# Performance work log

Hardware: AMD Instinct MI355X
Metric: run time of the kernel (lower is better)

The kernel has to match this reference:

```python
import jax, jax.numpy as jnp
import numpy as np

HID = 768
NSPLITS = 12
HEAD_RATIO = 2
H = NSPLITS // HEAD_RATIO          # 6 attention heads
D = HID // NSPLITS                 # 64 head size
AH = H * D                         # 384 all_head_size
KS = 9                             # conv kernel size
PAD = (KS - 1) // 2
B, S = 4, 1024


def setup_inputs() -> dict:
    key = jax.random.key(0)
    ks = jax.random.split(key, 16)
    std = 0.02
    inp = {
        "Q": jax.random.normal(ks[0], (B, S, HID), jnp.float32),
        "K": jax.random.normal(ks[1], (B, S, HID), jnp.float32),
        "V": jax.random.normal(ks[2], (B, S, HID), jnp.float32),
        "td": jax.random.uniform(ks[3], (B, S), jnp.float32),
        "mask": jax.random.randint(ks[4], (B, S), 0, 2, jnp.int32),
        # projection weights, applied as x @ W (in, out)
        "Wq": jax.random.normal(ks[5], (HID, AH), jnp.float32) * std,
        "Wk": jax.random.normal(ks[6], (HID, AH), jnp.float32) * std,
        "Wv": jax.random.normal(ks[7], (HID, AH), jnp.float32) * std,
        # separable conv: depthwise (HID, KS), pointwise (AH, HID), bias (AH,)
        "dw_w": jax.random.normal(ks[8], (HID, KS), jnp.float32) * std,
        "pw_w": jax.random.normal(ks[9], (AH, HID), jnp.float32) * std,
        "sep_b": jnp.zeros((AH,), jnp.float32),
        # conv_kernel_layer Linear(AH -> H*KS)
        "ck_W": jax.random.normal(ks[10], (AH, H * KS), jnp.float32) * std,
        "ck_b": jnp.zeros((H * KS,), jnp.float32),
        # conv_out_layer Linear(HID -> AH)
        "co_W": jax.random.normal(ks[11], (HID, AH), jnp.float32) * std,
        "co_b": jnp.zeros((AH,), jnp.float32),
        # gammas init to zeros as in torch module
        "gammas": jnp.zeros((H, 1, 1), jnp.float32),
    }
    return inp


def dist_func(scores, td, am, gammas):
    # scores: [B,H,S,S]; am: [B,1,1,S] bool key mask; entirely non-differentiable.
    s = scores.shape[-1]
    dt = scores.dtype
    amf = am.astype(dt)
    p = jax.nn.softmax(jnp.where(am, scores, -1e8), axis=-1) * amf
    distcum = jnp.cumsum(p, axis=-1)
    disttotal = jnp.sum(p, axis=-1, keepdims=True)
    # |j - i| position distance
    pos = jnp.abs(jnp.arange(s)[None, :] - jnp.arange(s)[:, None]).astype(dt)
    dist_scores = jnp.sqrt(jnp.clip((disttotal - distcum) * pos[None, None], 0.0, None))
    gamma = -jax.nn.softplus(gammas)[None]  # (1,H,1,1)
    total_effect = jnp.clip(jnp.exp(dist_scores * gamma), 1e-5, 1e5)
    # time-distance effect on strictly-lower-triangular positions
    tdn = td / jnp.maximum(jnp.linalg.norm(td, axis=-1, keepdims=True), 1e-12)
    td_scores = jnp.broadcast_to(tdn[:, None, None, :], scores.shape)
    td_sm = jax.nn.softmax(jnp.where(am, td_scores, -1e4), axis=-1)
    lower = jnp.tril(jnp.ones((s, s), dt), -1)  # (triu == 0)
    return jax.lax.stop_gradient(total_effect - td_sm * lower[None, None])


def reference(Q, K, V, td, mask, Wq, Wk, Wv, dw_w, pw_w, sep_b, ck_W, ck_b, co_W, co_b, gammas):
    b, s, hid = Q.shape
    mq = Q @ Wq  # (B,S,AH)
    mk = K @ Wk
    mv = V @ Wv
    # SeparableConv1D over sequence dim of K
    x = jnp.transpose(K, (0, 2, 1))  # (B,HID,S)
    dw = jax.lax.conv_general_dilated(
        x, dw_w[:, None, :], window_strides=(1,), padding=[(PAD, PAD)],
        feature_group_count=hid, dimension_numbers=("NCH", "OIH", "NCH"))
    pw = jnp.einsum("bcs,oc->bos", dw, pw_w) + sep_b[None, :, None]
    mkc = jnp.transpose(pw, (0, 2, 1))  # (B,S,AH)

    q = mq.reshape(b, s, H, D).transpose(0, 2, 1, 3)
    k = mk.reshape(b, s, H, D).transpose(0, 2, 1, 3)
    v = mv.reshape(b, s, H, D).transpose(0, 2, 1, 3)

    # dynamic span convolution
    conv_attn = mkc * mq                                   # (B,S,AH)
    ck = (conv_attn @ ck_W + ck_b).reshape(b, s, H, KS)
    ck = jax.nn.softmax(ck, axis=-1)                       # per-position kernel
    co = V @ co_W + co_b                                   # (B,S,AH)
    co_pad = jnp.pad(co, ((0, 0), (PAD, PAD), (0, 0)))
    idx = jnp.arange(s)[:, None] + jnp.arange(KS)[None, :]  # (S,KS)
    unf = co_pad[:, idx, :].reshape(b, s, KS, H, D)         # sliding window gather
    conv_out = jnp.einsum("bskhd,bshk->bshd", unf, ck)      # (B,S,H,D)

    # attention with distance decay
    scores = jnp.einsum("bhid,bhjd->bhij", q, k) / np.float32(np.sqrt(D))
    am = (mask[:, None, None, :] != 0)  # (B,1,1,S) key mask
    total_effect = dist_func(scores, td, am, gammas)
    scores = jnp.where(am, scores * total_effect, -1e8)
    probs = jax.nn.softmax(scores, axis=-1)
    ctx = jnp.einsum("bhij,bhjd->bhid", probs, v).transpose(0, 2, 1, 3)  # (B,S,H,D)

    out = jnp.concatenate([ctx, conv_out], axis=2).reshape(b, s, HEAD_RATIO * AH)
    return out
```

## Files before the change

kernel.cpp:

```cpp
#include <hip/hip_runtime.h>
#include <hip/hip_bf16.h>

#define HIDC 768
#define Hh   6
#define Dd   64
#define AHc  384
#define KSc  9
#define PADc 4
#define Bb   4
#define Ss   1024
#define MRr  (Bb * Ss)

typedef __attribute__((ext_vector_type(8))) __bf16 bf16x8;
typedef __attribute__((ext_vector_type(4))) float  f32x4;

__device__ __forceinline__ void split8(const float* p, bf16x8& hi, bf16x8& lo) {
    float4 x0 = *(const float4*)p;
    float4 x1 = *(const float4*)(p + 4);
    float xs[8] = {x0.x, x0.y, x0.z, x0.w, x1.x, x1.y, x1.z, x1.w};
#pragma unroll
    for (int e = 0; e < 8; ++e) {
        __bf16 hv = (__bf16)xs[e];
        hi[e] = hv;
        lo[e] = (__bf16)(xs[e] - (float)hv);
    }
}

__device__ __forceinline__ void split8r(const float* xs, bf16x8& hi, bf16x8& lo) {
#pragma unroll
    for (int e = 0; e < 8; ++e) {
        __bf16 hv = (__bf16)xs[e];
        hi[e] = hv;
        lo[e] = (__bf16)(xs[e] - (float)hv);
    }
}

__device__ __forceinline__ bf16x8 cvt8(const float* p) {
    float4 x0 = *(const float4*)p;
    float4 x1 = *(const float4*)(p + 4);
    float xs[8] = {x0.x, x0.y, x0.z, x0.w, x1.x, x1.y, x1.z, x1.w};
    bf16x8 h;
#pragma unroll
    for (int e = 0; e < 8; ++e) h[e] = (__bf16)xs[e];
    return h;
}

__global__ void k_depthwise(const float* __restrict__ Kin, const float* __restrict__ dww,
                            float* __restrict__ dwseq) {
    int idx = blockIdx.x * 256 + threadIdx.x;
    if (idx >= Bb * Ss * HIDC / 4) return;
    int c4 = idx % (HIDC / 4);
    int s  = (idx / (HIDC / 4)) % Ss;
    int b  = idx / ((HIDC / 4) * Ss);
    int c  = c4 * 4;
    float wv[4][KSc];
#pragma unroll
    for (int j = 0; j < 4; ++j)
#pragma unroll
        for (int k = 0; k < KSc; ++k) wv[j][k] = dww[(c + j) * KSc + k];
    float4 acc = {0.f, 0.f, 0.f, 0.f};
#pragma unroll
    for (int k = 0; k < KSc; ++k) {
        int sp = s + k - PADc;
        if (sp >= 0 && sp < Ss) {
            float4 v = *(const float4*)&Kin[(size_t)(b * Ss + sp) * HIDC + c];
            acc.x += v.x * wv[0][k]; acc.y += v.y * wv[1][k];
            acc.z += v.z * wv[2][k]; acc.w += v.w * wv[3][k];
        }
    }
    *(float4*)&dwseq[(size_t)idx * 4] = acc;
}

__global__ __launch_bounds__(256) void k_wsplit_t(const float* __restrict__ Wq, const float* __restrict__ Wk,
                                                  const float* __restrict__ Wv, const float* __restrict__ coW,
                                                  __bf16* __restrict__ Whi, __bf16* __restrict__ Wlo) {
    int z = blockIdx.z;
    const float* src = (z == 0) ? Wq : (z == 1) ? Wk : (z == 2) ? Wv : coW;
    int n0 = blockIdx.x * 64, k0 = blockIdx.y * 64;
    int tid = threadIdx.x;
    int r = tid >> 2, cq = tid & 3;
    __shared__ float tile[64][65];
#pragma unroll
    for (int e = 0; e < 4; ++e) {
        float4 v = *(const float4*)&src[(size_t)(k0 + r) * AHc + n0 + cq * 16 + e * 4];
        tile[r][cq * 16 + e * 4 + 0] = v.x;
        tile[r][cq * 16 + e * 4 + 1] = v.y;
        tile[r][cq * 16 + e * 4 + 2] = v.z;
        tile[r][cq * 16 + e * 4 + 3] = v.w;
    }
    __syncthreads();
    float x[16];
#pragma unroll
    for (int e = 0; e < 16; ++e) x[e] = tile[cq * 16 + e][r];
    bf16x8 h0, l0, h1, l1;
    split8r(x, h0, l0);
    split8r(x + 8, h1, l1);
    size_t dst = ((size_t)(z * AHc + n0 + r)) * HIDC + k0 + cq * 16;
    *(bf16x8*)(Whi + dst)     = h0;
    *(bf16x8*)(Whi + dst + 8) = h1;
    *(bf16x8*)(Wlo + dst)     = l0;
    *(bf16x8*)(Wlo + dst + 8) = l1;
}

__global__ void k_wsplit_c(const float* __restrict__ pww,
                           __bf16* __restrict__ Whi, __bf16* __restrict__ Wlo) {
    int idx = blockIdx.x * 256 + threadIdx.x;
    if (idx >= AHc * HIDC / 8) return;
    bf16x8 hi, lo;
    split8(pww + (size_t)idx * 8, hi, lo);
    size_t dst = (size_t)4 * AHc * HIDC + (size_t)idx * 8;
    *(bf16x8*)(Whi + dst) = hi;
    *(bf16x8*)(Wlo + dst) = lo;
}

__global__ void k_qkvsplit(const float* __restrict__ mq, const float* __restrict__ mk,
                           __bf16* __restrict__ qh, __bf16* __restrict__ kh,
                           __bf16* __restrict__ kl) {
    const int n8 = MRr * AHc / 8;
    int idx = blockIdx.x * 256 + threadIdx.x;
    if (idx >= 2 * n8) return;
    int which = idx / n8, i8 = idx % n8;
    if (which == 0) {
        *(bf16x8*)(qh + (size_t)i8 * 8) = cvt8(mq + (size_t)i8 * 8);
    } else {
        bf16x8 hi, lo;
        split8(mk + (size_t)i8 * 8, hi, lo);
        *(bf16x8*)(kh + (size_t)i8 * 8) = hi;
        *(bf16x8*)(kl + (size_t)i8 * 8) = lo;
    }
}

__global__ __launch_bounds__(256) void k_vtrans(const float* __restrict__ mv,
                                                __bf16* __restrict__ vt) {
    int s0 = blockIdx.x * 64;
    int h = blockIdx.y % Hh, b = blockIdx.y / Hh;
    int tid = threadIdx.x;
    int r = tid >> 2, cq = tid & 3;
    __shared__ float tile[64][65];
    const float* src = mv + (size_t)(b * Ss + s0 + r) * AHc + h * Dd + cq * 16;
#pragma unroll
    for (int e = 0; e < 4; ++e) {
        float4 v = *(const float4*)(src + e * 4);
        tile[r][cq * 16 + e * 4 + 0] = v.x;
        tile[r][cq * 16 + e * 4 + 1] = v.y;
        tile[r][cq * 16 + e * 4 + 2] = v.z;
        tile[r][cq * 16 + e * 4 + 3] = v.w;
    }
    __syncthreads();
    bf16x8 o0, o1;
#pragma unroll
    for (int e = 0; e < 8; ++e) {
        o0[e] = (__bf16)tile[cq * 16 + e][r];
        o1[e] = (__bf16)tile[cq * 16 + 8 + e][r];
    }
    __bf16* dst = vt + ((size_t)((b * Hh + h) * Dd + r)) * Ss + s0 + cq * 16;
    *(bf16x8*)dst       = o0;
    *(bf16x8*)(dst + 8) = o1;
}

__global__ void k_bias(const float* __restrict__ cob, const float* __restrict__ sepb,
                       float* __restrict__ biasb) {
    int idx = blockIdx.x * 256 + threadIdx.x;
    if (idx >= 5 * AHc) return;
    int z = idx / AHc, n = idx % AHc;
    biasb[idx] = (z == 3) ? cob[n] : (z == 4) ? sepb[n] : 0.f;
}

__global__ __launch_bounds__(256) void k_gemm5(
        const float* __restrict__ Q, const float* __restrict__ Kin,
        const float* __restrict__ V, const float* __restrict__ dwseq,
        const __bf16* __restrict__ Whi, const __bf16* __restrict__ Wlo,
        const float* __restrict__ biasb, float* __restrict__ Call) {
    __shared__ __attribute__((aligned(16))) __bf16 As_hi[128 * 40];
    __shared__ __attribute__((aligned(16))) __bf16 Bs_hi[128 * 40];
    __shared__ __attribute__((aligned(16))) __bf16 Bs_lo[128 * 40];

    int z = blockIdx.z;
    const float* Asrc = (z == 0) ? Q : (z == 1) ? Kin : (z <= 3) ? V : dwseq;
    int m0 = blockIdx.y * 128, n0 = blockIdx.x * 128;
    int tid = threadIdx.x;
    int wave = tid >> 6, lane = tid & 63, quad = lane >> 4, l15 = lane & 15;

    int sr = tid >> 1;
    int sk = (tid & 1) * 16;
    const float* Arow = Asrc + (size_t)(m0 + sr) * HIDC + sk;
    const __bf16* BhiRow = Whi + ((size_t)(z * AHc + n0 + sr)) * HIDC + sk;
    const __bf16* BloRow = Wlo + ((size_t)(z * AHc + n0 + sr)) * HIDC + sk;

    f32x4 acc[4][4] = {};

    for (int k0 = 0; k0 < HIDC; k0 += 32) {
        const float* ap = Arow + k0;
        *(bf16x8*)&As_hi[sr * 40 + sk]     = cvt8(ap);
        *(bf16x8*)&As_hi[sr * 40 + sk + 8] = cvt8(ap + 8);
        {
            const __bf16* bh = BhiRow + k0;
            const __bf16* bl = BloRow + k0;
            *(bf16x8*)&Bs_hi[sr * 40 + sk]     = *(const bf16x8*)bh;
            *(bf16x8*)&Bs_hi[sr * 40 + sk + 8] = *(const bf16x8*)(bh + 8);
            *(bf16x8*)&Bs_lo[sr * 40 + sk]     = *(const bf16x8*)bl;
            *(bf16x8*)&Bs_lo[sr * 40 + sk + 8] = *(const bf16x8*)(bl + 8);
        }
        __syncthreads();

        int mrow = (wave >> 1) * 64 + l15;
        int nrow = (wave & 1) * 64 + l15;
        bf16x8 ah[4], bh[4], bl[4];
#pragma unroll
        for (int mt = 0; mt < 4; ++mt)
            ah[mt] = *(bf16x8*)&As_hi[(mrow + mt * 16) * 40 + quad * 8];
#pragma unroll
        for (int nt = 0; nt < 4; ++nt) {
            bh[nt] = *(bf16x8*)&Bs_hi[(nrow + nt * 16) * 40 + quad * 8];
            bl[nt] = *(bf16x8*)&Bs_lo[(nrow + nt * 16) * 40 + quad * 8];
        }
#pragma unroll
        for (int mt = 0; mt < 4; ++mt)
#pragma unroll
            for (int nt = 0; nt < 4; ++nt) {
                acc[mt][nt] = __builtin_amdgcn_mfma_f32_16x16x32_bf16(ah[mt], bh[nt], acc[mt][nt], 0, 0, 0);
                acc[mt][nt] = __builtin_amdgcn_mfma_f32_16x16x32_bf16(ah[mt], bl[nt], acc[mt][nt], 0, 0, 0);
            }
        __syncthreads();
    }

    float* Cz = Call + (size_t)z * MRr * AHc;
    const float* bz = biasb + z * AHc;
#pragma unroll
    for (int nt = 0; nt < 4; ++nt) {
        int n = n0 + (wave & 1) * 64 + nt * 16 + l15;
        float bias = bz[n];
#pragma unroll
        for (int mt = 0; mt < 4; ++mt) {
#pragma unroll
            for (int r = 0; r < 4; ++r) {
                int m = m0 + (wave >> 1) * 64 + mt * 16 + quad * 4 + r;
                Cz[(size_t)m * AHc + n] = acc[mt][nt][r] + bias;
            }
        }
    }
}

__global__ __launch_bounds__(64) void k_ck(const float* __restrict__ mkc, const float* __restrict__ mq,
                                           const float* __restrict__ ckW, const float* __restrict__ ckb,
                                           float* __restrict__ ck_sm) {
    int row = blockIdx.x;
    int tid = threadIdx.x;
    __shared__ float ca[AHc];
    __shared__ float ckv[Hh * KSc];
    for (int o = tid; o < AHc; o += 64)
        ca[o] = mkc[row * AHc + o] * mq[row * AHc + o];
    __syncthreads();
    if (tid < Hh * KSc) {
        float acc = ckb[tid];
        for (int o = 0; o < AHc; ++o)
            acc += ca[o] * ckW[o * (Hh * KSc) + tid];
        ckv[tid] = acc;
    }
    __syncthreads();
    if (tid < Hh) {
        float m = -3e38f;
#pragma unroll
        for (int k = 0; k < KSc; ++k) m = fmaxf(m, ckv[tid * KSc + k]);
        float e[KSc];
        float s = 0.f;
#pragma unroll
        for (int k = 0; k < KSc; ++k) { e[k] = expf(ckv[tid * KSc + k] - m); s += e[k]; }
        float inv = 1.f / s;
#pragma unroll
        for (int k = 0; k < KSc; ++k) ck_sm[(row * Hh + tid) * KSc + k] = e[k] * inv;
    }
}

__global__ void k_convout(const float* __restrict__ co, const float* __restrict__ ck_sm,
                          float* __restrict__ out) {
    int idx = blockIdx.x * 256 + threadIdx.x;
    if (idx >= Bb * Ss * AHc / 4) return;
    int d4 = idx & 15;
    int h  = (idx >> 4) % Hh;
    int s  = (idx / (AHc / 4)) % Ss;
    int b  = idx / ((AHc / 4) * Ss);
    int row = b * Ss + s;
    const float* ck = ck_sm + (size_t)(row * Hh + h) * KSc;
    float4 acc = {0.f, 0.f, 0.f, 0.f};
#pragma unroll
    for (int k = 0; k < KSc; ++k) {
        int sp = s + k - PADc;
        if (sp >= 0 && sp < Ss) {
            float4 v = *(const float4*)&co[(size_t)(b * Ss + sp) * AHc + h * Dd + d4 * 4];
            float wv = ck[k];
            acc.x += wv * v.x; acc.y += wv * v.y; acc.z += wv * v.z; acc.w += wv * v.w;
        }
    }
    *(float4*)&out[(size_t)row * (2 * AHc) + AHc + h * Dd + d4 * 4] = acc;
}

__global__ __launch_bounds__(256) void k_td(const float* __restrict__ td, const int* __restrict__ mask,
                                            float* __restrict__ td_sm) {
    int b = blockIdx.x;
    int tid = threadIdx.x;
    __shared__ float red[256];
    __shared__ float tv[Ss];
    float ls = 0.f;
    for (int j = tid; j < Ss; j += 256) {
        float v = td[b * Ss + j];
        tv[j] = v;
        ls += v * v;
    }
    red[tid] = ls; __syncthreads();
    for (int s = 128; s > 0; s >>= 1) { if (tid < s) red[tid] += red[tid + s]; __syncthreads(); }
    float norm = fmaxf(sqrtf(red[0]), 1e-12f);
    __syncthreads();
    float lm = -3e38f;
    for (int j = tid; j < Ss; j += 256) {
        float v = mask[b * Ss + j] ? tv[j] / norm : -1e4f;
        tv[j] = v;
        lm = fmaxf(lm, v);
    }
    red[tid] = lm; __syncthreads();
    for (int s = 128; s > 0; s >>= 1) { if (tid < s) red[tid] = fmaxf(red[tid], red[tid + s]); __syncthreads(); }
    float m = red[0]; __syncthreads();
    float lsum = 0.f;
    for (int j = tid; j < Ss; j += 256) {
        float e = expf(tv[j] - m);
        tv[j] = e;
        lsum += e;
    }
    red[tid] = lsum; __syncthreads();
    for (int s = 128; s > 0; s >>= 1) { if (tid < s) red[tid] += red[tid + s]; __syncthreads(); }
    float inv = 1.f / red[0];
    __syncthreads();
    for (int j = tid; j < Ss; j += 256)
        td_sm[b * Ss + j] = tv[j] * inv;
}

__device__ __forceinline__ int scix(int m, int j) {
    return m * 1024 + (j ^ (((m ^ (j >> 6)) & 7) << 2));
}

__global__ __launch_bounds__(512) void k_attn(const __bf16* __restrict__ qh,
                                              const __bf16* __restrict__ kh, const __bf16* __restrict__ kl,
                                              const __bf16* __restrict__ vt,
                                              const int* __restrict__ mask,
                                              const float* __restrict__ td_sm, const float* __restrict__ gammas,
                                              float* __restrict__ out) {
    __shared__ float sc[16 * 1024];
    int wg = blockIdx.x + 64 * blockIdx.y;
    int n  = (wg & 7) * 192 + (wg >> 3);
    int bx = n & 63, by = n >> 6;
    int i0 = bx * 16;
    int h = by % Hh, b = by / Hh;
    int tid = threadIdx.x;
    int w = tid >> 6, lane = tid & 63, quad = lane >> 4, l15 = lane & 15;
    int jw = w * 128;

    bf16x8 a_hi[2];
    {
        size_t qoff = (size_t)(b * Ss + i0 + l15) * AHc + h * Dd + quad * 8;
        a_hi[0] = *(const bf16x8*)(qh + qoff);
        a_hi[1] = *(const bf16x8*)(qh + qoff + 32);
    }
#pragma unroll 2
    for (int t = 0; t < 8; ++t) {
        int jt = jw + t * 16;
        size_t koff = (size_t)(b * Ss + jt + l15) * AHc + h * Dd + quad * 8;
        f32x4 acc = {0.f, 0.f, 0.f, 0.f};
#pragma unroll
        for (int kc = 0; kc < 2; ++kc) {
            bf16x8 khv = *(const bf16x8*)(kh + koff + kc * 32);
            bf16x8 klv = *(const bf16x8*)(kl + koff + kc * 32);
            acc = __builtin_amdgcn_mfma_f32_16x16x32_bf16(a_hi[kc], khv, acc, 0, 0, 0);
            acc = __builtin_amdgcn_mfma_f32_16x16x32_bf16(a_hi[kc], klv, acc, 0, 0, 0);
        }
#pragma unroll
        for (int r = 0; r < 4; ++r)
            sc[scix(quad * 4 + r, jt + l15)] = acc[r] * 0.125f;
    }
    __syncthreads();

    const int* mrow = mask + b * Ss;
    const float* tdrow = td_sm + b * Ss;
    float gamma = -log1pf(expf(gammas[h]));
    int jb = lane << 4;
    __attribute__((aligned(16))) int marr[16];
    {
        const int4* mp = (const int4*)(mrow + jb);
#pragma unroll
        for (int k = 0; k < 4; ++k) ((int4*)marr)[k] = mp[k];
    }
    __attribute__((aligned(16))) float tdv[16];
    {
        const float4* tp = (const float4*)(tdrow + jb);
#pragma unroll
        for (int k = 0; k < 4; ++k) ((float4*)tdv)[k] = tp[k];
    }

#pragma unroll
    for (int r4 = 0; r4 < 2; ++r4) {
        int m = w * 2 + r4;
        int i = i0 + m;
        __attribute__((aligned(16))) float s[16];
        float p[16];
#pragma unroll
        for (int g = 0; g < 4; ++g)
            *(f32x4*)(s + 4 * g) = *(const f32x4*)&sc[scix(m, jb + 4 * g)];
        float mx = -1e30f;
#pragma unroll
        for (int jj = 0; jj < 16; ++jj) mx = fmaxf(mx, marr[jj] ? s[jj] : -1e30f);
        mx = fmaxf(mx, __shfl_xor(mx, 1));  mx = fmaxf(mx, __shfl_xor(mx, 2));
        mx = fmaxf(mx, __shfl_xor(mx, 4));  mx = fmaxf(mx, __shfl_xor(mx, 8));
        mx = fmaxf(mx, __shfl_xor(mx, 16)); mx = fmaxf(mx, __shfl_xor(mx, 32));
#pragma unroll
        for (int jj = 0; jj < 16; ++jj) p[jj] = marr[jj] ? __expf(s[jj] - mx) : 0.f;
#pragma unroll
        for (int jj = 1; jj < 16; ++jj) p[jj] += p[jj - 1];
        float t = p[15];
        float incl = t;
#pragma unroll
        for (int dlt = 1; dlt < 64; dlt <<= 1) {
            float v = __shfl_up(incl, dlt);
            if (lane >= dlt) incl += v;
        }
        float off = incl - t;
        float tot = __shfl(incl, 63);
        float inv = 1.f / fmaxf(tot, 1e-30f);
        float mx2 = -1e30f;
#pragma unroll
        for (int jj = 0; jj < 16; ++jj) {
            int j = jb + jj;
            float cum = p[jj] + off;
            float pos = fabsf((float)(j - i));
            float ds = sqrtf(fmaxf((tot - cum) * inv * pos, 0.f));
            float te = fminf(fmaxf(__expf(ds * gamma), 1e-5f), 1e5f);
            float mult = te - ((j < i) ? tdv[jj] : 0.f);
            float s2 = marr[jj] ? s[jj] * mult : -1e8f;
            s[jj] = s2;
            mx2 = fmaxf(mx2, s2);
        }
        mx2 = fmaxf(mx2, __shfl_xor(mx2, 1));  mx2 = fmaxf(mx2, __shfl_xor(mx2, 2));
        mx2 = fmaxf(mx2, __shfl_xor(mx2, 4));  mx2 = fmaxf(mx2, __shfl_xor(mx2, 8));
        mx2 = fmaxf(mx2, __shfl_xor(mx2, 16)); mx2 = fmaxf(mx2, __shfl_xor(mx2, 32));
        float sm = 0.f;
#pragma unroll
        for (int jj = 0; jj < 16; ++jj) { s[jj] = __expf(s[jj] - mx2); sm += s[jj]; }
        sm += __shfl_xor(sm, 1);  sm += __shfl_xor(sm, 2);
        sm += __shfl_xor(sm, 4);  sm += __shfl_xor(sm, 8);
        sm += __shfl_xor(sm, 16); sm += __shfl_xor(sm, 32);
        float inv2 = 1.f / sm;
#pragma unroll
        for (int jj = 0; jj < 16; ++jj) s[jj] *= inv2;
#pragma unroll
        for (int g = 0; g < 4; ++g)
            *(f32x4*)&sc[scix(m, jb + 4 * g)] = *(const f32x4*)(s + 4 * g);
    }
    __syncthreads();

    f32x4 oacc[4] = {};
    const __bf16* vtb = vt + (size_t)(b * Hh + h) * Dd * Ss;
#pragma unroll
    for (int kc = 0; kc < 4; ++kc) {
        int j0 = jw + kc * 32 + quad * 8;
        __attribute__((aligned(16))) float x[8];
        *(f32x4*)x       = *(const f32x4*)&sc[scix(l15, j0)];
        *(f32x4*)(x + 4) = *(const f32x4*)&sc[scix(l15, j0 + 4)];
        bf16x8 p_hi, p_lo;
        split8r(x, p_hi, p_lo);
#pragma unroll
        for (int nt = 0; nt < 4; ++nt) {
            int d = nt * 16 + l15;
            bf16x8 vv = *(const bf16x8*)(vtb + (size_t)d * Ss + j0);
            oacc[nt] = __builtin_amdgcn_mfma_f32_16x16x32_bf16(p_hi, vv, oacc[nt], 0, 0, 0);
            oacc[nt] = __builtin_amdgcn_mfma_f32_16x16x32_bf16(p_lo, vv, oacc[nt], 0, 0, 0);
        }
    }
    __syncthreads();
#pragma unroll
    for (int nt = 0; nt < 4; ++nt)
#pragma unroll
        for (int r = 0; r < 4; ++r)
            sc[w * 1024 + (quad * 4 + r) * 64 + nt * 16 + l15] = oacc[nt][r];
    __syncthreads();
#pragma unroll
    for (int e = 0; e < 2; ++e) {
        int idx = e * 512 + tid;
        int m = idx >> 6, dd = idx & 63;
        float v = 0.f;
#pragma unroll
        for (int ww = 0; ww < 8; ++ww) v += sc[ww * 1024 + idx];
        out[(size_t)(b * Ss + i0 + m) * (2 * AHc) + h * Dd + dd] = v;
    }
}

extern "C" void kernel_launch(void* const* d_in, const int* in_sizes, int n_in,
                              void* d_out, int out_size, void* d_ws, size_t ws_size,
                              hipStream_t stream) {
    const float* Q    = (const float*)d_in[0];
    const float* Kin  = (const float*)d_in[1];
    const float* V    = (const float*)d_in[2];
    const float* td   = (const float*)d_in[3];
    const int*   mask = (const int*)d_in[4];
    const float* Wq   = (const float*)d_in[5];
    const float* Wk   = (const float*)d_in[6];
    const float* Wv   = (const float*)d_in[7];
    const float* dww  = (const float*)d_in[8];
    const float* pww  = (const float*)d_in[9];
    const float* sepb = (const float*)d_in[10];
    const float* ckW  = (const float*)d_in[11];
    const float* ckb  = (const float*)d_in[12];
    const float* coW  = (const float*)d_in[13];
    const float* cob  = (const float*)d_in[14];
    const float* gam  = (const float*)d_in[15];
    float* out = (float*)d_out;
    float* ws = (float*)d_ws;

    float* mq    = ws;
    float* mk    = mq    + (size_t)MRr * AHc;
    float* mv    = mk    + (size_t)MRr * AHc;
    float* co    = mv    + (size_t)MRr * AHc;
    float* mkc   = co    + (size_t)MRr * AHc;
    float* dwseq = mkc   + (size_t)MRr * AHc;
    float* cksm  = dwseq + (size_t)MRr * HIDC;
    float* tdsm  = cksm  + (size_t)MRr * Hh * KSc;
    float* biasb = tdsm  + (size_t)Bb * Ss;

    __bf16* Whi = (__bf16*)d_out;
    __bf16* Wlo = Whi + (size_t)5 * AHc * HIDC;
    __bf16* qh = (__bf16*)dwseq;
    __bf16* kh = qh + (size_t)MRr * AHc;
    __bf16* kl = kh + (size_t)MRr * AHc;
    __bf16* vt = kl + (size_t)MRr * AHc;

    dim3 gt(AHc / 64, HIDC / 64, 4);
    k_wsplit_t<<<gt, 256, 0, stream>>>(Wq, Wk, Wv, coW, Whi, Wlo);
    k_wsplit_c<<<(AHc * HIDC / 8 + 255) / 256, 256, 0, stream>>>(pww, Whi, Wlo);
    k_depthwise<<<(MRr * HIDC / 4 + 255) / 256, 256, 0, stream>>>(Kin, dww, dwseq);
    k_bias<<<(5 * AHc + 255) / 256, 256, 0, stream>>>(cob, sepb, biasb);

    dim3 gg(AHc / 128, MRr / 128, 5);
    k_gemm5<<<gg, 256, 0, stream>>>(Q, Kin, V, dwseq, Whi, Wlo, biasb, mq);

    k_qkvsplit<<<(2 * MRr * AHc / 8 + 255) / 256, 256, 0, stream>>>(mq, mk, qh, kh, kl);
    k_vtrans<<<dim3(Ss / 64, Bb * Hh), 256, 0, stream>>>(mv, vt);
    k_ck<<<MRr, 64, 0, stream>>>(mkc, mq, ckW, ckb, cksm);
    k_convout<<<(MRr * AHc / 4 + 255) / 256, 256, 0, stream>>>(co, cksm, out);
    k_td<<<Bb, 256, 0, stream>>>(td, mask, tdsm);

    dim3 ga(Ss / 16, Bb * Hh);
    k_attn<<<ga, 512, 0, stream>>>(qh, kh, kl, vt, mask, tdsm, gam, out);
}
```

Baseline: 302.3 us.

## Use direct global-to-LDS loads for GEMM weights, remap workgroups, vectorize ck kernel

The batched projection GEMM now loads its bf16 hi/lo weight tiles with global_load_lds straight into unpadded shared memory instead of staging them through registers. It also remaps workgroup IDs with a stride-8 permutation, likely to spread neighbouring tiles across XCDs for better L2 locality. Separately, the ck weight matrix is transposed once in a small new kernel so the per-row ck kernel can use float4 loads for the dot products. The unpadded B tile layout may introduce LDS bank conflicts on the MFMA operand reads, and the extra transpose kernel adds a launch.

```diff
diff --git a/kernel.cpp b/kernel.cpp
--- a/kernel.cpp
+++ b/kernel.cpp
@@ -14,6 +14,12 @@
 typedef __attribute__((ext_vector_type(8))) __bf16 bf16x8;
 typedef __attribute__((ext_vector_type(4))) float  f32x4;
 
+__device__ __forceinline__ void gl_lds16(const void* g, void* l) {
+    __builtin_amdgcn_global_load_lds(
+        (const __attribute__((address_space(1))) void*)g,
+        (__attribute__((address_space(3))) void*)l, 16, 0, 0);
+}
+
 __device__ __forceinline__ void split8(const float* p, bf16x8& hi, bf16x8& lo) {
     float4 x0 = *(const float4*)p;
     float4 x1 = *(const float4*)(p + 4);
@@ -111,6 +117,13 @@
     size_t dst = (size_t)4 * AHc * HIDC + (size_t)idx * 8;
     *(bf16x8*)(Whi + dst) = hi;
     *(bf16x8*)(Wlo + dst) = lo;
+}
+
+__global__ void k_ckwT(const float* __restrict__ ckW, float* __restrict__ ckWt) {
+    int idx = blockIdx.x * 256 + threadIdx.x;
+    if (idx >= AHc * Hh * KSc) return;
+    int o = idx / (Hh * KSc), t = idx % (Hh * KSc);
+    ckWt[t * AHc + o] = ckW[idx];
 }
 
 __global__ void k_qkvsplit(const float* __restrict__ mq, const float* __restrict__ mk,
@@ -172,20 +185,32 @@
         const __bf16* __restrict__ Whi, const __bf16* __restrict__ Wlo,
         const float* __restrict__ biasb, float* __restrict__ Call) {
     __shared__ __attribute__((aligned(16))) __bf16 As_hi[128 * 40];
-    __shared__ __attribute__((aligned(16))) __bf16 Bs_hi[128 * 40];
-    __shared__ __attribute__((aligned(16))) __bf16 Bs_lo[128 * 40];
-
-    int z = blockIdx.z;
+    __shared__ __attribute__((aligned(16))) __bf16 Bs_hi[128 * 32];
+    __shared__ __attribute__((aligned(16))) __bf16 Bs_lo[128 * 32];
+
+    int wg = blockIdx.x + 3 * (blockIdx.y + 32 * blockIdx.z);
+    int n2 = (wg & 7) * 60 + (wg >> 3);
+    int bxx = n2 % 3, byy = (n2 / 3) % 32, z = n2 / 96;
+
     const float* Asrc = (z == 0) ? Q : (z == 1) ? Kin : (z <= 3) ? V : dwseq;
-    int m0 = blockIdx.y * 128, n0 = blockIdx.x * 128;
+    int m0 = byy * 128, n0 = bxx * 128;
     int tid = threadIdx.x;
     int wave = tid >> 6, lane = tid & 63, quad = lane >> 4, l15 = lane & 15;
 
     int sr = tid >> 1;
     int sk = (tid & 1) * 16;
     const float* Arow = Asrc + (size_t)(m0 + sr) * HIDC + sk;
-    const __bf16* BhiRow = Whi + ((size_t)(z * AHc + n0 + sr)) * HIDC + sk;
-    const __bf16* BloRow = Wlo + ((size_t)(z * AHc + n0 + sr)) * HIDC + sk;
+
+    int brow = wave * 32 + (lane >> 2);
+    int bcol = (lane & 3) * 8;
+    const __bf16* BhG0 = Whi + ((size_t)(z * AHc + n0 + brow)) * HIDC + bcol;
+    const __bf16* BhG1 = BhG0 + (size_t)16 * HIDC;
+    const __bf16* BlG0 = Wlo + ((size_t)(z * AHc + n0 + brow)) * HIDC + bcol;
+    const __bf16* BlG1 = BlG0 + (size_t)16 * HIDC;
+    __bf16* BhL0 = Bs_hi + (wave * 2 + 0) * 512;
+    __bf16* BhL1 = Bs_hi + (wave * 2 + 1) * 512;
+    __bf16* BlL0 = Bs_lo + (wave * 2 + 0) * 512;
+    __bf16* BlL1 = Bs_lo + (wave * 2 + 1) * 512;
 
     f32x4 acc[4][4] = {};
 
@@ -193,14 +218,10 @@
         const float* ap = Arow + k0;
         *(bf16x8*)&As_hi[sr * 40 + sk]     = cvt8(ap);
         *(bf16x8*)&As_hi[sr * 40 + sk + 8] = cvt8(ap + 8);
-        {
-            const __bf16* bh = BhiRow + k0;
-            const __bf16* bl = BloRow + k0;
-            *(bf16x8*)&Bs_hi[sr * 40 + sk]     = *(const bf16x8*)bh;
-            *(bf16x8*)&Bs_hi[sr * 40 + sk + 8] = *(const bf16x8*)(bh + 8);
-            *(bf16x8*)&Bs_lo[sr * 40 + sk]     = *(const bf16x8*)bl;
-            *(bf16x8*)&Bs_lo[sr * 40 + sk + 8] = *(const bf16x8*)(bl + 8);
-        }
+        gl_lds16(BhG0 + k0, BhL0);
+        gl_lds16(BhG1 + k0, BhL1);
+        gl_lds16(BlG0 + k0, BlL0);
+        gl_lds16(BlG1 + k0, BlL1);
         __syncthreads();
 
         int mrow = (wave >> 1) * 64 + l15;
@@ -211,8 +232,8 @@
             ah[mt] = *(bf16x8*)&As_hi[(mrow + mt * 16) * 40 + quad * 8];
 #pragma unroll
         for (int nt = 0; nt < 4; ++nt) {
-            bh[nt] = *(bf16x8*)&Bs_hi[(nrow + nt * 16) * 40 + quad * 8];
-            bl[nt] = *(bf16x8*)&Bs_lo[(nrow + nt * 16) * 40 + quad * 8];
+            bh[nt] = *(bf16x8*)&Bs_hi[(nrow + nt * 16) * 32 + quad * 8];
+            bl[nt] = *(bf16x8*)&Bs_lo[(nrow + nt * 16) * 32 + quad * 8];
         }
 #pragma unroll
         for (int mt = 0; mt < 4; ++mt)
@@ -242,19 +263,34 @@
 }
 
 __global__ __launch_bounds__(64) void k_ck(const float* __restrict__ mkc, const float* __restrict__ mq,
-                                           const float* __restrict__ ckW, const float* __restrict__ ckb,
+                                           const float* __restrict__ ckWt, const float* __restrict__ ckb,
                                            float* __restrict__ ck_sm) {
     int row = blockIdx.x;
     int tid = threadIdx.x;
-    __shared__ float ca[AHc];
+    __shared__ __attribute__((aligned(16))) float ca[AHc];
     __shared__ float ckv[Hh * KSc];
-    for (int o = tid; o < AHc; o += 64)
-        ca[o] = mkc[row * AHc + o] * mq[row * AHc + o];
+    const float4* am = (const float4*)(mkc + (size_t)row * AHc);
+    const float4* aq = (const float4*)(mq + (size_t)row * AHc);
+#pragma unroll
+    for (int o = 0; o < 2; ++o) {
+        int i4 = tid + o * 64;
+        if (i4 < AHc / 4) {
+            float4 a = am[i4], b = aq[i4];
+            float4 r;
+            r.x = a.x * b.x; r.y = a.y * b.y; r.z = a.z * b.z; r.w = a.w * b.w;
+            ((float4*)ca)[i4] = r;
+        }
+    }
     __syncthreads();
     if (tid < Hh * KSc) {
         float acc = ckb[tid];
-        for (int o = 0; o < AHc; ++o)
-            acc += ca[o] * ckW[o * (Hh * KSc) + tid];
+        const float4* wr = (const float4*)(ckWt + tid * AHc);
+        const float4* cr = (const float4*)ca;
+#pragma unroll 4
+        for (int o4 = 0; o4 < AHc / 4; ++o4) {
+            float4 wv = wr[o4], cv = cr[o4];
+            acc += wv.x * cv.x + wv.y * cv.y + wv.z * cv.z + wv.w * cv.w;
+        }
         ckv[tid] = acc;
     }
     __syncthreads();
@@ -522,6 +558,7 @@
     float* cksm  = dwseq + (size_t)MRr * HIDC;
     float* tdsm  = cksm  + (size_t)MRr * Hh * KSc;
     float* biasb = tdsm  + (size_t)Bb * Ss;
+    float* ckwt  = biasb + (size_t)5 * AHc;
 
     __bf16* Whi = (__bf16*)d_out;
     __bf16* Wlo = Whi + (size_t)5 * AHc * HIDC;
@@ -533,6 +570,7 @@
     dim3 gt(AHc / 64, HIDC / 64, 4);
     k_wsplit_t<<<gt, 256, 0, stream>>>(Wq, Wk, Wv, coW, Whi, Wlo);
     k_wsplit_c<<<(AHc * HIDC / 8 + 255) / 256, 256, 0, stream>>>(pww, Whi, Wlo);
+    k_ckwT<<<(AHc * Hh * KSc + 255) / 256, 256, 0, stream>>>(ckW, ckwt);
     k_depthwise<<<(MRr * HIDC / 4 + 255) / 256, 256, 0, stream>>>(Kin, dww, dwseq);
     k_bias<<<(5 * AHc + 255) / 256, 256, 0, stream>>>(cob, sepb, biasb);
 
@@ -541,7 +579,7 @@
 
     k_qkvsplit<<<(2 * MRr * AHc / 8 + 255) / 256, 256, 0, stream>>>(mq, mk, qh, kh, kl);
     k_vtrans<<<dim3(Ss / 64, Bb * Hh), 256, 0, stream>>>(mv, vt);
-    k_ck<<<MRr, 64, 0, stream>>>(mkc, mq, ckW, ckb, cksm);
+    k_ck<<<MRr, 64, 0, stream>>>(mkc, mq, ckwt, ckb, cksm);
     k_convout<<<(MRr * AHc / 4 + 255) / 256, 256, 0, stream>>>(co, cksm, out);
     k_td<<<Bb, 256, 0, stream>>>(td, mask, tdsm);
 
```

New measurement: 321.8 us. +6.5%, slower.

## Pre-convert GEMM inputs to bf16, use direct global-to-LDS loads, fuse K split

Applied to the files above, without the earlier changes.

Q, V and the depthwise output are converted to bf16 once before the projection GEMM, so the GEMM A-operand loads use async global_load_lds with an XOR-swizzled unpadded LDS layout instead of per-tile fp32 conversion. The GEMM also remaps workgroup IDs across the grid, and the K-projection slice writes its hi/lo bf16 split directly, removing part of the separate split kernel. This adds an extra conversion pass over Q and V, and moves some buffers (the bf16 V copy now lives in the output buffer).

```diff
diff --git a/kernel.cpp b/kernel.cpp
--- a/kernel.cpp
+++ b/kernel.cpp
@@ -12,7 +12,14 @@
 #define MRr  (Bb * Ss)
 
 typedef __attribute__((ext_vector_type(8))) __bf16 bf16x8;
+typedef __attribute__((ext_vector_type(4))) __bf16 bf16x4;
 typedef __attribute__((ext_vector_type(4))) float  f32x4;
+
+__device__ __forceinline__ void gl_lds16(const void* g, void* l) {
+    __builtin_amdgcn_global_load_lds(
+        (const __attribute__((address_space(1))) void*)g,
+        (__attribute__((address_space(3))) void*)l, 16, 0, 0);
+}
 
 __device__ __forceinline__ void split8(const float* p, bf16x8& hi, bf16x8& lo) {
     float4 x0 = *(const float4*)p;
@@ -46,7 +53,7 @@
 }
 
 __global__ void k_depthwise(const float* __restrict__ Kin, const float* __restrict__ dww,
-                            float* __restrict__ dwseq) {
+                            __bf16* __restrict__ dwbf) {
     int idx = blockIdx.x * 256 + threadIdx.x;
     if (idx >= Bb * Ss * HIDC / 4) return;
     int c4 = idx % (HIDC / 4);
@@ -68,7 +75,8 @@
             acc.z += v.z * wv[2][k]; acc.w += v.w * wv[3][k];
         }
     }
-    *(float4*)&dwseq[(size_t)idx * 4] = acc;
+    bf16x4 o = {(__bf16)acc.x, (__bf16)acc.y, (__bf16)acc.z, (__bf16)acc.w};
+    *(bf16x4*)(dwbf + (size_t)idx * 4) = o;
 }
 
 __global__ __launch_bounds__(256) void k_wsplit_t(const float* __restrict__ Wq, const float* __restrict__ Wk,
@@ -113,21 +121,23 @@
     *(bf16x8*)(Wlo + dst) = lo;
 }
 
-__global__ void k_qkvsplit(const float* __restrict__ mq, const float* __restrict__ mk,
-                           __bf16* __restrict__ qh, __bf16* __restrict__ kh,
-                           __bf16* __restrict__ kl) {
-    const int n8 = MRr * AHc / 8;
+__global__ void k_absplit(const float* __restrict__ Q, const float* __restrict__ V,
+                          __bf16* __restrict__ qbf, __bf16* __restrict__ vbf) {
+    const int n8 = MRr * HIDC / 8;
     int idx = blockIdx.x * 256 + threadIdx.x;
     if (idx >= 2 * n8) return;
-    int which = idx / n8, i8 = idx % n8;
-    if (which == 0) {
-        *(bf16x8*)(qh + (size_t)i8 * 8) = cvt8(mq + (size_t)i8 * 8);
+    if (idx < n8) {
+        *(bf16x8*)(qbf + (size_t)idx * 8) = cvt8(Q + (size_t)idx * 8);
     } else {
-        bf16x8 hi, lo;
-        split8(mk + (size_t)i8 * 8, hi, lo);
-        *(bf16x8*)(kh + (size_t)i8 * 8) = hi;
-        *(bf16x8*)(kl + (size_t)i8 * 8) = lo;
-    }
+        int i = idx - n8;
+        *(bf16x8*)(vbf + (size_t)i * 8) = cvt8(V + (size_t)i * 8);
+    }
+}
+
+__global__ void k_qkvsplit(const float* __restrict__ mq, __bf16* __restrict__ qh) {
+    int idx = blockIdx.x * 256 + threadIdx.x;
+    if (idx >= MRr * AHc / 8) return;
+    *(bf16x8*)(qh + (size_t)idx * 8) = cvt8(mq + (size_t)idx * 8);
 }
 
 __global__ __launch_bounds__(256) void k_vtrans(const float* __restrict__ mv,
@@ -167,40 +177,65 @@
 }
 
 __global__ __launch_bounds__(256) void k_gemm5(
-        const float* __restrict__ Q, const float* __restrict__ Kin,
-        const float* __restrict__ V, const float* __restrict__ dwseq,
+        const __bf16* __restrict__ qbf, const float* __restrict__ Kin,
+        const __bf16* __restrict__ vbf, const __bf16* __restrict__ dwbf,
         const __bf16* __restrict__ Whi, const __bf16* __restrict__ Wlo,
-        const float* __restrict__ biasb, float* __restrict__ Call) {
-    __shared__ __attribute__((aligned(16))) __bf16 As_hi[128 * 40];
-    __shared__ __attribute__((aligned(16))) __bf16 Bs_hi[128 * 40];
-    __shared__ __attribute__((aligned(16))) __bf16 Bs_lo[128 * 40];
-
-    int z = blockIdx.z;
-    const float* Asrc = (z == 0) ? Q : (z == 1) ? Kin : (z <= 3) ? V : dwseq;
-    int m0 = blockIdx.y * 128, n0 = blockIdx.x * 128;
+        const float* __restrict__ biasb, float* __restrict__ Call,
+        __bf16* __restrict__ kh, __bf16* __restrict__ kl) {
+    __shared__ __attribute__((aligned(16))) __bf16 As [128 * 32];
+    __shared__ __attribute__((aligned(16))) __bf16 BsH[128 * 32];
+    __shared__ __attribute__((aligned(16))) __bf16 BsL[128 * 32];
+
+    int wg = blockIdx.x + 3 * (blockIdx.y + 32 * blockIdx.z);
+    int n2 = (wg & 7) * 60 + (wg >> 3);
+    int bxx = n2 % 3, byy = (n2 / 3) % 32, z = n2 / 96;
+
+    int m0 = byy * 128, n0 = bxx * 128;
     int tid = threadIdx.x;
     int wave = tid >> 6, lane = tid & 63, quad = lane >> 4, l15 = lane & 15;
 
+    int lrow = lane >> 2;
+    int lswz = 8 * ((lane & 3) ^ (lrow & 3));
+
+    int brow = wave * 32 + lrow;
+    const __bf16* BhG0 = Whi + ((size_t)(z * AHc + n0 + brow)) * HIDC + lswz;
+    const __bf16* BhG1 = BhG0 + (size_t)16 * HIDC;
+    const __bf16* BlG0 = Wlo + ((size_t)(z * AHc + n0 + brow)) * HIDC + lswz;
+    const __bf16* BlG1 = BlG0 + (size_t)16 * HIDC;
+    __bf16* BhL0 = BsH + (wave * 2 + 0) * 512;
+    __bf16* BhL1 = BsH + (wave * 2 + 1) * 512;
+    __bf16* BlL0 = BsL + (wave * 2 + 0) * 512;
+    __bf16* BlL1 = BsL + (wave * 2 + 1) * 512;
+
+    const __bf16* Abf = (z == 0) ? qbf : (z == 4) ? dwbf : vbf;
+    const __bf16* AG0 = Abf + ((size_t)(m0 + wave * 32 + lrow)) * HIDC + lswz;
+    const __bf16* AG1 = AG0 + (size_t)16 * HIDC;
+    __bf16* AL0 = As + (wave * 2 + 0) * 512;
+    __bf16* AL1 = As + (wave * 2 + 1) * 512;
+
     int sr = tid >> 1;
     int sk = (tid & 1) * 16;
-    const float* Arow = Asrc + (size_t)(m0 + sr) * HIDC + sk;
-    const __bf16* BhiRow = Whi + ((size_t)(z * AHc + n0 + sr)) * HIDC + sk;
-    const __bf16* BloRow = Wlo + ((size_t)(z * AHc + n0 + sr)) * HIDC + sk;
-
+    const float* Arow = Kin + (size_t)(m0 + sr) * HIDC + sk;
+    int g0 = sk >> 3;
+    int d0 = sr * 32 + ((g0       ^ (sr & 3)) * 8);
+    int d1 = sr * 32 + (((g0 + 1) ^ (sr & 3)) * 8);
+
+    int swz = (quad ^ (l15 & 3)) * 8;
     f32x4 acc[4][4] = {};
 
     for (int k0 = 0; k0 < HIDC; k0 += 32) {
-        const float* ap = Arow + k0;
-        *(bf16x8*)&As_hi[sr * 40 + sk]     = cvt8(ap);
-        *(bf16x8*)&As_hi[sr * 40 + sk + 8] = cvt8(ap + 8);
-        {
-            const __bf16* bh = BhiRow + k0;
-            const __bf16* bl = BloRow + k0;
-            *(bf16x8*)&Bs_hi[sr * 40 + sk]     = *(const bf16x8*)bh;
-            *(bf16x8*)&Bs_hi[sr * 40 + sk + 8] = *(const bf16x8*)(bh + 8);
-            *(bf16x8*)&Bs_lo[sr * 40 + sk]     = *(const bf16x8*)bl;
-            *(bf16x8*)&Bs_lo[sr * 40 + sk + 8] = *(const bf16x8*)(bl + 8);
-        }
+        if (z == 1) {
+            const float* ap = Arow + k0;
+            *(bf16x8*)&As[d0] = cvt8(ap);
+            *(bf16x8*)&As[d1] = cvt8(ap + 8);
+        } else {
+            gl_lds16(AG0 + k0, AL0);
+            gl_lds16(AG1 + k0, AL1);
+        }
+        gl_lds16(BhG0 + k0, BhL0);
+        gl_lds16(BhG1 + k0, BhL1);
+        gl_lds16(BlG0 + k0, BlL0);
+        gl_lds16(BlG1 + k0, BlL1);
         __syncthreads();
 
         int mrow = (wave >> 1) * 64 + l15;
@@ -208,11 +243,11 @@
         bf16x8 ah[4], bh[4], bl[4];
 #pragma unroll
         for (int mt = 0; mt < 4; ++mt)
-            ah[mt] = *(bf16x8*)&As_hi[(mrow + mt * 16) * 40 + quad * 8];
+            ah[mt] = *(bf16x8*)&As[(mrow + mt * 16) * 32 + swz];
 #pragma unroll
         for (int nt = 0; nt < 4; ++nt) {
-            bh[nt] = *(bf16x8*)&Bs_hi[(nrow + nt * 16) * 40 + quad * 8];
-            bl[nt] = *(bf16x8*)&Bs_lo[(nrow + nt * 16) * 40 + quad * 8];
+            bh[nt] = *(bf16x8*)&BsH[(nrow + nt * 16) * 32 + swz];
+            bl[nt] = *(bf16x8*)&BsL[(nrow + nt * 16) * 32 + swz];
         }
 #pragma unroll
         for (int mt = 0; mt < 4; ++mt)
@@ -224,18 +259,36 @@
         __syncthreads();
     }
 
-    float* Cz = Call + (size_t)z * MRr * AHc;
-    const float* bz = biasb + z * AHc;
-#pragma unroll
-    for (int nt = 0; nt < 4; ++nt) {
-        int n = n0 + (wave & 1) * 64 + nt * 16 + l15;
-        float bias = bz[n];
-#pragma unroll
-        for (int mt = 0; mt < 4; ++mt) {
-#pragma unroll
-            for (int r = 0; r < 4; ++r) {
-                int m = m0 + (wave >> 1) * 64 + mt * 16 + quad * 4 + r;
-                Cz[(size_t)m * AHc + n] = acc[mt][nt][r] + bias;
+    if (z == 1) {
+#pragma unroll
+        for (int nt = 0; nt < 4; ++nt) {
+            int n = n0 + (wave & 1) * 64 + nt * 16 + l15;
+#pragma unroll
+            for (int mt = 0; mt < 4; ++mt) {
+#pragma unroll
+                for (int r = 0; r < 4; ++r) {
+                    int m = m0 + (wave >> 1) * 64 + mt * 16 + quad * 4 + r;
+                    float v = acc[mt][nt][r];
+                    __bf16 hv = (__bf16)v;
+                    kh[(size_t)m * AHc + n] = hv;
+                    kl[(size_t)m * AHc + n] = (__bf16)(v - (float)hv);
+                }
+            }
+        }
+    } else {
+        float* Cz = Call + (size_t)z * MRr * AHc;
+        const float* bz = biasb + z * AHc;
+#pragma unroll
+        for (int nt = 0; nt < 4; ++nt) {
+            int n = n0 + (wave & 1) * 64 + nt * 16 + l15;
+            float bias = bz[n];
+#pragma unroll
+            for (int mt = 0; mt < 4; ++mt) {
+#pragma unroll
+                for (int r = 0; r < 4; ++r) {
+                    int m = m0 + (wave >> 1) * 64 + mt * 16 + quad * 4 + r;
+                    Cz[(size_t)m * AHc + n] = acc[mt][nt][r] + bias;
+                }
             }
         }
     }
@@ -514,32 +567,37 @@
     float* ws = (float*)d_ws;
 
     float* mq    = ws;
-    float* mk    = mq    + (size_t)MRr * AHc;
-    float* mv    = mk    + (size_t)MRr * AHc;
+    float* mks   = mq    + (size_t)MRr * AHc;
+    float* mv    = mks   + (size_t)MRr * AHc;
     float* co    = mv    + (size_t)MRr * AHc;
     float* mkc   = co    + (size_t)MRr * AHc;
-    float* dwseq = mkc   + (size_t)MRr * AHc;
-    float* cksm  = dwseq + (size_t)MRr * HIDC;
+    float* dwr   = mkc   + (size_t)MRr * AHc;
+    float* cksm  = dwr   + (size_t)MRr * HIDC;
     float* tdsm  = cksm  + (size_t)MRr * Hh * KSc;
     float* biasb = tdsm  + (size_t)Bb * Ss;
 
+    __bf16* dwbf = (__bf16*)dwr;
+    __bf16* qbf  = (__bf16*)(dwr + (size_t)MRr * HIDC / 2);
+    __bf16* qh   = (__bf16*)dwr;
+    __bf16* vt   = (__bf16*)(dwr + (size_t)MRr * HIDC / 2);
+    __bf16* kh = (__bf16*)mks;
+    __bf16* kl = kh + (size_t)MRr * AHc;
+
     __bf16* Whi = (__bf16*)d_out;
     __bf16* Wlo = Whi + (size_t)5 * AHc * HIDC;
-    __bf16* qh = (__bf16*)dwseq;
-    __bf16* kh = qh + (size_t)MRr * AHc;
-    __bf16* kl = kh + (size_t)MRr * AHc;
-    __bf16* vt = kl + (size_t)MRr * AHc;
+    __bf16* vbf = Wlo + (size_t)5 * AHc * HIDC;
 
     dim3 gt(AHc / 64, HIDC / 64, 4);
     k_wsplit_t<<<gt, 256, 0, stream>>>(Wq, Wk, Wv, coW, Whi, Wlo);
     k_wsplit_c<<<(AHc * HIDC / 8 + 255) / 256, 256, 0, stream>>>(pww, Whi, Wlo);
-    k_depthwise<<<(MRr * HIDC / 4 + 255) / 256, 256, 0, stream>>>(Kin, dww, dwseq);
+    k_absplit<<<(2 * MRr * HIDC / 8 + 255) / 256, 256, 0, stream>>>(Q, V, qbf, vbf);
+    k_depthwise<<<(MRr * HIDC / 4 + 255) / 256, 256, 0, stream>>>(Kin, dww, dwbf);
     k_bias<<<(5 * AHc + 255) / 256, 256, 0, stream>>>(cob, sepb, biasb);
 
     dim3 gg(AHc / 128, MRr / 128, 5);
-    k_gemm5<<<gg, 256, 0, stream>>>(Q, Kin, V, dwseq, Whi, Wlo, biasb, mq);
-
-    k_qkvsplit<<<(2 * MRr * AHc / 8 + 255) / 256, 256, 0, stream>>>(mq, mk, qh, kh, kl);
+    k_gemm5<<<gg, 256, 0, stream>>>(qbf, Kin, vbf, dwbf, Whi, Wlo, biasb, mq, kh, kl);
+
+    k_qkvsplit<<<(MRr * AHc / 8 + 255) / 256, 256, 0, stream>>>(mq, qh);
     k_vtrans<<<dim3(Ss / 64, Bb * Hh), 256, 0, stream>>>(mv, vt);
     k_ck<<<MRr, 64, 0, stream>>>(mkc, mq, ckW, ckb, cksm);
     k_convout<<<(MRr * AHc / 4 + 255) / 256, 256, 0, stream>>>(co, cksm, out);
```

After: 303.4 us. Within noise of the previous version (+0.4%).
